# Performance work log

Measured on AMD Instinct MI355X. Metric: run time of the kernel, lower is better.

The kernel has to match this reference:

```python
import jax, jax.numpy as jnp
import numpy as np

N = 50000   # nodes
E = 200000  # edges (avg degree ~4, pose-graph-like sparsity)
F_IN = 512
NEG_SLOPE = 0.01  # F.leaky_relu default


def _softmax_aggr(src_feat, dst, num_nodes):
    # torch_geometric SoftmaxAggregation(t=1): per-destination, per-feature
    # alpha = softmax(x_j), out = sum_j alpha * x_j
    m = jax.ops.segment_max(src_feat, dst, num_segments=num_nodes)  # [N,F]
    m = jnp.where(jnp.isfinite(m), m, 0.0)  # empty segments -> -inf guard
    e = jnp.exp(src_feat - m[dst])                                   # [E,F]
    denom = jax.ops.segment_sum(e, dst, num_segments=num_nodes)      # [N,F]
    num = jax.ops.segment_sum(e * src_feat, dst, num_segments=num_nodes)
    return num / jnp.maximum(denom, 1e-16)  # 0 for isolated nodes


def setup_inputs() -> dict:
    key = jax.random.key(0)
    ks = jax.random.split(key, 9)
    inp = {
        "x": jax.random.normal(ks[0], (N, F_IN), dtype=jnp.float32),
        "W1_rel": jax.random.normal(ks[1], (513, 256), dtype=jnp.float32) * 0.04,
        "b1_rel": jnp.zeros((256,), dtype=jnp.float32),
        "W1_root": jax.random.normal(ks[2], (513, 256), dtype=jnp.float32) * 0.04,
        "W2_rel": jax.random.normal(ks[3], (257, 64), dtype=jnp.float32) * 0.06,
        "b2_rel": jnp.zeros((64,), dtype=jnp.float32),
        "W2_root": jax.random.normal(ks[4], (257, 64), dtype=jnp.float32) * 0.06,
        "Wp": jax.random.normal(ks[5], (65, 3), dtype=jnp.float32) * 0.1,
        "bp": jnp.zeros((3,), dtype=jnp.float32),
        "Wr": jax.random.normal(ks[6], (65, 4), dtype=jnp.float32) * 0.1,
        "br": jnp.zeros((4,), dtype=jnp.float32),
        "edge_index": jax.random.randint(ks[7], (2, E), 0, N, dtype=jnp.int64),
    }
    return inp


def reference(x, W1_rel, b1_rel, W1_root, W2_rel, b2_rel, W2_root,
              Wp, bp, Wr, br, edge_index):
    src, dst = edge_index[0], edge_index[1]
    node_index = jnp.arange(x.shape[0], dtype=x.dtype)[:, None]  # [N,1]

    # dropout is identity in eval mode
    h = jnp.concatenate([x, node_index], axis=1)  # [N,513]

    # GraphConv(513,256, aggr='softmax'): lin_rel(softmax_aggr(x_j)) + lin_root(x)
    agg1 = _softmax_aggr(h[src], dst, x.shape[0])               # [N,513]
    h = agg1 @ W1_rel + b1_rel + h @ W1_root                     # [N,256]
    h = jnp.where(h >= 0, h, NEG_SLOPE * h)

    h = jnp.concatenate([h, node_index], axis=1)  # [N,257]

    # GraphConv(257,64) default aggr='add'
    agg2 = jax.ops.segment_sum(h[src], dst, num_segments=x.shape[0])  # [N,257]
    h = agg2 @ W2_rel + b2_rel + h @ W2_root                           # [N,64]
    h = jnp.where(h >= 0, h, NEG_SLOPE * h)

    h = jnp.concatenate([h, node_index], axis=1)  # [N,65]

    position = h @ Wp + bp                         # [N,3]
    rotation = h @ Wr + br                         # [N,4]
    norm = jnp.linalg.norm(rotation, axis=1, keepdims=True)
    rotation = rotation / jnp.maximum(norm, 1e-12)  # F.normalize

    return jnp.concatenate([position, rotation], axis=1)  # [N,7]
```

## Files before the change

kernel.cpp:

```cpp
#include <hip/hip_runtime.h>

#define NNODES 50000
#define NEDGES 200000
#define NSCANB ((NNODES + 255) / 256)

typedef short  bf16x8 __attribute__((ext_vector_type(8)));
typedef float  f32x4  __attribute__((ext_vector_type(4)));
typedef unsigned int u32x4 __attribute__((ext_vector_type(4)));

__device__ __forceinline__ unsigned short f2bf(float f) {
    union { float f; unsigned int u; } c; c.f = f;
    unsigned int r = c.u + 0x7fffu + ((c.u >> 16) & 1u);
    return (unsigned short)(r >> 16);
}
__device__ __forceinline__ float bflo(unsigned int v) {
    union { unsigned int u; float f; } c; c.u = v << 16;
    return c.f;
}
__device__ __forceinline__ float bfhi(unsigned int v) {
    union { unsigned int u; float f; } c; c.u = v & 0xffff0000u;
    return c.f;
}

#define PREP_B1 (256 * 1024)
#define PREP_B2 (64 * 512)
#define PREP_XC (NNODES * 64)
__global__ __launch_bounds__(256) void k_prepcount(const float* __restrict__ x,
                                                   const float* __restrict__ W1_rel,
                                                   const float* __restrict__ W1_root,
                                                   const float* __restrict__ W2_rel,
                                                   const float* __restrict__ W2_root,
                                                   const int* __restrict__ ei,
                                                   int* __restrict__ deg,
                                                   unsigned short* __restrict__ Bt1,
                                                   unsigned short* __restrict__ Bt2,
                                                   unsigned short* __restrict__ xb) {
    const int gtid = blockIdx.x * 256 + threadIdx.x;
    const int GS = gridDim.x * 256;
    for (int e = gtid; e < NEDGES; e += GS) atomicAdd(&deg[ei[NEDGES + e]], 1);
    for (int i = gtid; i < PREP_B1; i += GS) {
        int n = i >> 10, k = i & 1023;
        float v = (k < 512) ? W1_rel[k * 256 + n] : W1_root[(k - 512) * 256 + n];
        Bt1[i] = f2bf(v);
    }
    for (int i = gtid; i < PREP_B2; i += GS) {
        int n = i >> 9, k = i & 511;
        float v = (k < 256) ? W2_rel[k * 64 + n] : W2_root[(k - 256) * 64 + n];
        Bt2[i] = f2bf(v);
    }
    for (int i = gtid; i < PREP_XC; i += GS) {
        int n = i >> 6, c8 = (i & 63) * 8;
        const float* xp = x + (size_t)n * 512 + c8;
        float4 a = *(const float4*)xp;
        float4 bb = *(const float4*)(xp + 4);
        unsigned short o[8];
        o[0] = f2bf(a.x); o[1] = f2bf(a.y); o[2] = f2bf(a.z); o[3] = f2bf(a.w);
        o[4] = f2bf(bb.x); o[5] = f2bf(bb.y); o[6] = f2bf(bb.z); o[7] = f2bf(bb.w);
        *(u32x4*)(xb + (size_t)n * 512 + c8) = *(const u32x4*)o;
    }
}

__global__ __launch_bounds__(256) void k_scanA(const int* __restrict__ deg,
                                               int* __restrict__ rs,
                                               int* __restrict__ partials) {
    __shared__ int sm[256];
    int t = threadIdx.x, i = blockIdx.x * 256 + t;
    int v = (i < NNODES) ? deg[i] : 0;
    sm[t] = v;
    __syncthreads();
#pragma unroll
    for (int off = 1; off < 256; off <<= 1) {
        int u = (t >= off) ? sm[t - off] : 0;
        __syncthreads();
        sm[t] += u;
        __syncthreads();
    }
    if (i < NNODES) rs[i] = sm[t] - v;
    if (t == 255) partials[blockIdx.x] = sm[255];
}

__global__ __launch_bounds__(256) void k_scanC2(int* __restrict__ rs,
                                                const int* __restrict__ partials,
                                                int* __restrict__ cursor) {
    __shared__ int sm[256];
    int t = threadIdx.x, b = blockIdx.x;
    sm[t] = (t < b && t < NSCANB) ? partials[t] : 0;
    __syncthreads();
#pragma unroll
    for (int off = 128; off; off >>= 1) {
        if (t < off) sm[t] += sm[t + off];
        __syncthreads();
    }
    int off0 = sm[0];
    int i = b * 256 + t;
    if (i < NNODES) {
        int rv = rs[i] + off0;
        rs[i] = rv;
        cursor[i] = rv;
    }
    if (i == 0) rs[NNODES] = NEDGES;
}

__global__ void k_scatter(const int* __restrict__ ei, int* __restrict__ cursor,
                          int* __restrict__ srcs) {
    int e = blockIdx.x * 256 + threadIdx.x;
    if (e < NEDGES) {
        int d = ei[NEDGES + e];
        int p = atomicAdd(&cursor[d], 1);
        srcs[p] = ei[e];
    }
}

__global__ __launch_bounds__(256) void k_agg1(const unsigned short* __restrict__ xb,
                                              const int* __restrict__ rs,
                                              const int* __restrict__ srcs,
                                              unsigned short* __restrict__ AggBuf) {
    int wv = threadIdx.x >> 6;
    int lane = threadIdx.x & 63;
    int n = blockIdx.x * 4 + wv;
    int e0 = rs[n], e1 = rs[n + 1];
    float nu[8], de[8];
#pragma unroll
    for (int j = 0; j < 8; ++j) { nu[j] = 0.f; de[j] = 0.f; }

    auto accum = [&](u32x4 r) {
#pragma unroll
        for (int p = 0; p < 4; ++p) {
            float v0 = bflo(r[p]), v1 = bfhi(r[p]);
            float E0 = __expf(v0), E1 = __expf(v1);
            de[2 * p] += E0; nu[2 * p] += E0 * v0;
            de[2 * p + 1] += E1; nu[2 * p + 1] += E1 * v1;
        }
    };

    int e = e0;
    for (; e + 3 < e1; e += 4) {
        int s0 = srcs[e], s1 = srcs[e + 1], s2 = srcs[e + 2], s3 = srcs[e + 3];
        u32x4 r0 = *(const u32x4*)(xb + (size_t)s0 * 512 + lane * 8);
        u32x4 r1 = *(const u32x4*)(xb + (size_t)s1 * 512 + lane * 8);
        u32x4 r2 = *(const u32x4*)(xb + (size_t)s2 * 512 + lane * 8);
        u32x4 r3 = *(const u32x4*)(xb + (size_t)s3 * 512 + lane * 8);
        accum(r0); accum(r1); accum(r2); accum(r3);
    }
    if (e + 1 < e1) {
        int s0 = srcs[e], s1 = srcs[e + 1];
        u32x4 r0 = *(const u32x4*)(xb + (size_t)s0 * 512 + lane * 8);
        u32x4 r1 = *(const u32x4*)(xb + (size_t)s1 * 512 + lane * 8);
        accum(r0); accum(r1);
        e += 2;
    }
    if (e < e1) {
        u32x4 r0 = *(const u32x4*)(xb + (size_t)srcs[e] * 512 + lane * 8);
        accum(r0);
    }
    unsigned short o[8];
#pragma unroll
    for (int j = 0; j < 8; ++j) o[j] = f2bf(nu[j] / fmaxf(de[j], 1e-16f));
    *(u32x4*)(AggBuf + (size_t)n * 512 + lane * 8) = *(const u32x4*)o;
}

__global__ __launch_bounds__(256) void k_agg2(const int* __restrict__ rs,
                                              const int* __restrict__ srcs,
                                              const unsigned short* __restrict__ H1,
                                              unsigned short* __restrict__ Seg) {
    int wv = threadIdx.x >> 6;
    int lane = threadIdx.x & 63;
    int n = blockIdx.x * 4 + wv;
    int e0 = rs[n], e1 = rs[n + 1];
    float a[4] = {0.f, 0.f, 0.f, 0.f};

    auto accum = [&](uint2 r) {
        a[0] += bflo(r.x); a[1] += bfhi(r.x);
        a[2] += bflo(r.y); a[3] += bfhi(r.y);
    };

    int e = e0;
    for (; e + 3 < e1; e += 4) {
        int s0 = srcs[e], s1 = srcs[e + 1], s2 = srcs[e + 2], s3 = srcs[e + 3];
        uint2 r0 = *(const uint2*)(H1 + (size_t)s0 * 256 + lane * 4);
        uint2 r1 = *(const uint2*)(H1 + (size_t)s1 * 256 + lane * 4);
        uint2 r2 = *(const uint2*)(H1 + (size_t)s2 * 256 + lane * 4);
        uint2 r3 = *(const uint2*)(H1 + (size_t)s3 * 256 + lane * 4);
        accum(r0); accum(r1); accum(r2); accum(r3);
    }
    if (e + 1 < e1) {
        int s0 = srcs[e], s1 = srcs[e + 1];
        uint2 r0 = *(const uint2*)(H1 + (size_t)s0 * 256 + lane * 4);
        uint2 r1 = *(const uint2*)(H1 + (size_t)s1 * 256 + lane * 4);
        accum(r0); accum(r1);
        e += 2;
    }
    if (e < e1) {
        uint2 r0 = *(const uint2*)(H1 + (size_t)srcs[e] * 256 + lane * 4);
        accum(r0);
    }
    uint2 o;
    o.x = (unsigned int)f2bf(a[0]) | ((unsigned int)f2bf(a[1]) << 16);
    o.y = (unsigned int)f2bf(a[2]) | ((unsigned int)f2bf(a[3]) << 16);
    *(uint2*)(Seg + (size_t)n * 256 + lane * 4) = o;
}

__global__ __launch_bounds__(256) void k_gemm1(const unsigned short* __restrict__ A1,
                                               const unsigned short* __restrict__ A2,
                                               const unsigned short* __restrict__ Bt,
                                               const int* __restrict__ rs,
                                               const int* __restrict__ srcs,
                                               const float* __restrict__ r1,
                                               const float* __restrict__ r2,
                                               const float* __restrict__ bias,
                                               unsigned short* __restrict__ outp) {
    constexpr int BM = 64, BN = 128, BK = 64;
    __shared__ __align__(16) unsigned short As[2][BM * BK];
    __shared__ __align__(16) unsigned short Bs[2][BN * BK];
    __shared__ float s1t[BM];

    const int tid = threadIdx.x;
    const int w = tid >> 6;
    const int lane = tid & 63;
    const int lm = lane & 15;
    const int quad = lane >> 4;
    const int wr = w >> 1;
    const int wc = w & 1;
    const int rowbase = blockIdx.y * BM;
    const int colbase = blockIdx.x * BN;
    const int wrow = wr * 32;
    const int wcol = wc * 64;

    const int rsub = lane >> 3;
    const int csw = (lane & 7) ^ rsub;

    f32x4 acc[2][4];
#pragma unroll
    for (int mi = 0; mi < 2; ++mi)
#pragma unroll
        for (int ni = 0; ni < 4; ++ni) acc[mi][ni] = (f32x4){0.f, 0.f, 0.f, 0.f};

    auto stage = [&](unsigned short* Asb, unsigned short* Bsb, int kt) {
        const unsigned short* Ab = (kt < 512) ? A1 : A2;
        int kof = (kt < 512) ? kt : kt - 512;
#pragma unroll
        for (int l = 0; l < 2; ++l) {
            int r = w * 16 + l * 8;
            int gr = rowbase + r + rsub;
            if (gr >= NNODES) gr = NNODES - 1;
            const unsigned short* gp = Ab + (size_t)gr * 512 + kof + csw * 8;
            __builtin_amdgcn_global_load_lds(
                (const __attribute__((address_space(1))) void*)gp,
                (__attribute__((address_space(3))) void*)(Asb + r * BK), 16, 0, 0);
        }
#pragma unroll
        for (int l = 0; l < 4; ++l) {
            int r = w * 32 + l * 8;
            const unsigned short* gp = Bt + (size_t)(colbase + r + rsub) * 1024 + kt + csw * 8;
            __builtin_amdgcn_global_load_lds(
                (const __attribute__((address_space(1))) void*)gp,
                (__attribute__((address_space(3))) void*)(Bsb + r * BK), 16, 0, 0);
        }
    };

    auto compute = [&](const unsigned short* Asb, const unsigned short* Bsb) {
#pragma unroll
        for (int kk = 0; kk < BK; kk += 32) {
            const int kidx = (kk >> 3) + quad;
            const int phys = kidx ^ (lm & 7);
            bf16x8 af[2], bfr[4];
#pragma unroll
            for (int mi = 0; mi < 2; ++mi)
                af[mi] = __builtin_bit_cast(bf16x8,
                    *(const u32x4*)(Asb + (wrow + mi * 16 + lm) * BK + phys * 8));
#pragma unroll
            for (int ni = 0; ni < 4; ++ni)
                bfr[ni] = __builtin_bit_cast(bf16x8,
                    *(const u32x4*)(Bsb + (wcol + ni * 16 + lm) * BK + phys * 8));
#pragma unroll
            for (int mi = 0; mi < 2; ++mi)
#pragma unroll
                for (int ni = 0; ni < 4; ++ni)
                    acc[mi][ni] = __builtin_amdgcn_mfma_f32_16x16x32_bf16(
                        af[mi], bfr[ni], acc[mi][ni], 0, 0, 0);
        }
    };

    stage(As[0], Bs[0], 0);
#pragma unroll 1
    for (int t = 0; t < 16; t += 2) {
        stage(As[1], Bs[1], (t + 1) * BK);
        asm volatile("s_waitcnt vmcnt(6)" ::: "memory");
        __builtin_amdgcn_s_barrier();
        __builtin_amdgcn_sched_barrier(0);
        compute(As[0], Bs[0]);
        __builtin_amdgcn_s_barrier();
        if (t + 2 < 16) {
            stage(As[0], Bs[0], (t + 2) * BK);
            asm volatile("s_waitcnt vmcnt(6)" ::: "memory");
        } else {
            asm volatile("s_waitcnt vmcnt(0)" ::: "memory");
        }
        __builtin_amdgcn_s_barrier();
        __builtin_amdgcn_sched_barrier(0);
        compute(As[1], Bs[1]);
        __builtin_amdgcn_s_barrier();
    }

    if (tid < BM) {
        int grow = rowbase + tid;
        float r_ = 0.f;
        if (grow < NNODES) {
            int e0 = rs[grow], e1 = rs[grow + 1];
            float m = -INFINITY, d = 0.f, q = 0.f;
            for (int e = e0; e < e1; ++e) {
                float v = (float)srcs[e];
                float nm = fmaxf(m, v);
                float sc = __expf(m - nm), ee = __expf(v - nm);
                d = d * sc + ee;
                q = q * sc + ee * v;
                m = nm;
            }
            r_ = q / fmaxf(d, 1e-16f);
        }
        s1t[tid] = r_;
    }
    __syncthreads();

#pragma unroll
    for (int ni = 0; ni < 4; ++ni) {
        int gc = colbase + wcol + ni * 16 + lm;
        float r1v = r1[gc], r2v = r2[gc], bv = bias[gc];
#pragma unroll
        for (int mi = 0; mi < 2; ++mi) {
#pragma unroll
            for (int r = 0; r < 4; ++r) {
                int lrow = wrow + mi * 16 + quad * 4 + r;
                int grow = rowbase + lrow;
                if (grow < NNODES) {
                    float v = acc[mi][ni][r] + s1t[lrow] * r1v + (float)grow * r2v + bv;
                    v = (v >= 0.f) ? v : 0.01f * v;
                    outp[(size_t)grow * 256 + gc] = f2bf(v);
                }
            }
        }
    }
}

__global__ __launch_bounds__(256) void k_gemm2h(const unsigned short* __restrict__ A1,
                                                const unsigned short* __restrict__ A2,
                                                const unsigned short* __restrict__ Bt,
                                                const int* __restrict__ rs,
                                                const int* __restrict__ srcs,
                                                const float* __restrict__ r1,
                                                const float* __restrict__ r2,
                                                const float* __restrict__ bias,
                                                const float* __restrict__ Wp,
                                                const float* __restrict__ bp,
                                                const float* __restrict__ Wr,
                                                const float* __restrict__ br,
                                                float* __restrict__ out) {
    constexpr int BM = 64, BN = 64, BK = 64;
    __shared__ __align__(16) unsigned short As[BM * BK];
    __shared__ __align__(16) unsigned short Bs[BN * BK];
    __shared__ float h2t[BM * 65];
    __shared__ float s1t[BM];

    const int tid = threadIdx.x;
    const int w = tid >> 6;
    const int lane = tid & 63;
    const int lm = lane & 15;
    const int quad = lane >> 4;
    const int rowbase = blockIdx.x * BM;
    const int wrow = w * 16;

    const int rsub = lane >> 3;
    const int csw = (lane & 7) ^ rsub;

    f32x4 acc[4];
#pragma unroll
    for (int ni = 0; ni < 4; ++ni) acc[ni] = (f32x4){0.f, 0.f, 0.f, 0.f};

    for (int kt = 0; kt < 512; kt += BK) {
        const unsigned short* Ab = (kt < 256) ? A1 : A2;
        int kof = (kt < 256) ? kt : kt - 256;
#pragma unroll
        for (int l = 0; l < 2; ++l) {
            int r = w * 16 + l * 8;
            int gr = rowbase + r + rsub;
            if (gr >= NNODES) gr = NNODES - 1;
            const unsigned short* gp = Ab + (size_t)gr * 256 + kof + csw * 8;
            __builtin_amdgcn_global_load_lds(
                (const __attribute__((address_space(1))) void*)gp,
                (__attribute__((address_space(3))) void*)(As + r * BK), 16, 0, 0);
        }
#pragma unroll
        for (int l = 0; l < 2; ++l) {
            int r = w * 16 + l * 8;
            const unsigned short* gp = Bt + (size_t)(r + rsub) * 512 + kt + csw * 8;
            __builtin_amdgcn_global_load_lds(
                (const __attribute__((address_space(1))) void*)gp,
                (__attribute__((address_space(3))) void*)(Bs + r * BK), 16, 0, 0);
        }
        __syncthreads();
#pragma unroll
        for (int kk = 0; kk < BK; kk += 32) {
            const int kidx = (kk >> 3) + quad;
            const int phys = kidx ^ (lm & 7);
            bf16x8 af;
            af = __builtin_bit_cast(bf16x8,
                *(const u32x4*)(As + (wrow + lm) * BK + phys * 8));
            bf16x8 bfr[4];
#pragma unroll
            for (int ni = 0; ni < 4; ++ni)
                bfr[ni] = __builtin_bit_cast(bf16x8,
                    *(const u32x4*)(Bs + (ni * 16 + lm) * BK + phys * 8));
#pragma unroll
            for (int ni = 0; ni < 4; ++ni)
                acc[ni] = __builtin_amdgcn_mfma_f32_16x16x32_bf16(
                    af, bfr[ni], acc[ni], 0, 0, 0);
        }
        __syncthreads();
    }

    if (tid < BM) {
        int grow = rowbase + tid;
        float si = 0.f;
        if (grow < NNODES) {
            int e0 = rs[grow], e1 = rs[grow + 1];
            for (int e = e0; e < e1; ++e) si += (float)srcs[e];
        }
        s1t[tid] = si;
    }
    __syncthreads();

#pragma unroll
    for (int ni = 0; ni < 4; ++ni) {
        int gc = ni * 16 + lm;
        float r1v = r1[gc], r2v = r2[gc], bv = bias[gc];
#pragma unroll
        for (int r = 0; r < 4; ++r) {
            int lrow = wrow + quad * 4 + r;
            int grow = rowbase + lrow;
            float v = acc[ni][r] + s1t[lrow] * r1v + (float)grow * r2v + bv;
            v = (v >= 0.f) ? v : 0.01f * v;
            h2t[lrow * 65 + gc] = v;
        }
    }
    __syncthreads();

    if (tid < BM) {
        int grow = rowbase + tid;
        if (grow < NNODES) {
            const float* hv = h2t + tid * 65;
            float idx = (float)grow;
            float p0 = 0.f, p1 = 0.f, p2 = 0.f;
            float r0 = 0.f, r1a = 0.f, r2a = 0.f, r3 = 0.f;
#pragma unroll 8
            for (int c = 0; c < 64; ++c) {
                float v = hv[c];
                p0 += v * Wp[c * 3 + 0];
                p1 += v * Wp[c * 3 + 1];
                p2 += v * Wp[c * 3 + 2];
                r0 += v * Wr[c * 4 + 0];
                r1a += v * Wr[c * 4 + 1];
                r2a += v * Wr[c * 4 + 2];
                r3 += v * Wr[c * 4 + 3];
            }
            p0 += idx * Wp[64 * 3 + 0] + bp[0];
            p1 += idx * Wp[64 * 3 + 1] + bp[1];
            p2 += idx * Wp[64 * 3 + 2] + bp[2];
            r0 += idx * Wr[64 * 4 + 0] + br[0];
            r1a += idx * Wr[64 * 4 + 1] + br[1];
            r2a += idx * Wr[64 * 4 + 2] + br[2];
            r3 += idx * Wr[64 * 4 + 3] + br[3];
            float nrm = fmaxf(sqrtf(r0 * r0 + r1a * r1a + r2a * r2a + r3 * r3), 1e-12f);
            float* op = out + (size_t)grow * 7;
            op[0] = p0; op[1] = p1; op[2] = p2;
            op[3] = r0 / nrm; op[4] = r1a / nrm; op[5] = r2a / nrm; op[6] = r3 / nrm;
        }
    }
}

extern "C" void kernel_launch(void* const* d_in, const int* in_sizes, int n_in,
                              void* d_out, int out_size, void* d_ws, size_t ws_size,
                              hipStream_t stream) {
    const float* x       = (const float*)d_in[0];
    const float* W1_rel  = (const float*)d_in[1];
    const float* b1      = (const float*)d_in[2];
    const float* W1_root = (const float*)d_in[3];
    const float* W2_rel  = (const float*)d_in[4];
    const float* b2      = (const float*)d_in[5];
    const float* W2_root = (const float*)d_in[6];
    const float* Wp      = (const float*)d_in[7];
    const float* bp      = (const float*)d_in[8];
    const float* Wr      = (const float*)d_in[9];
    const float* br      = (const float*)d_in[10];
    const int*   ei      = (const int*)d_in[11];
    float* out = (float*)d_out;

    char* ws = (char*)d_ws;
    size_t off = 0;
    auto alloc = [&](size_t bytes) {
        size_t o = off;
        off = (off + bytes + 255) & ~(size_t)255;
        return (void*)(ws + o);
    };
    int*   deg       = (int*)alloc(NNODES * 4);
    int*   cursor    = (int*)alloc(NNODES * 4);
    int*   row_start = (int*)alloc((NNODES + 1) * 4);
    int*   srcs      = (int*)alloc(NEDGES * 4);
    int*   partials  = (int*)alloc(NSCANB * 4);
    unsigned short* xb     = (unsigned short*)alloc((size_t)NNODES * 512 * 2);
    unsigned short* AggBuf = (unsigned short*)alloc((size_t)NNODES * 512 * 2);
    unsigned short* H1     = (unsigned short*)alloc((size_t)NNODES * 256 * 2);
    unsigned short* Seg    = (unsigned short*)alloc((size_t)NNODES * 256 * 2);
    unsigned short* Bt1    = (unsigned short*)alloc(256 * 1024 * 2);
    unsigned short* Bt2    = (unsigned short*)alloc(64 * 512 * 2);

    hipMemsetAsync(deg, 0, NNODES * 4, stream);

    k_prepcount<<<2048, 256, 0, stream>>>(
        x, W1_rel, W1_root, W2_rel, W2_root, ei, deg, Bt1, Bt2, xb);

    k_scanA<<<NSCANB, 256, 0, stream>>>(deg, row_start, partials);
    k_scanC2<<<NSCANB, 256, 0, stream>>>(row_start, partials, cursor);
    k_scatter<<<(NEDGES + 255) / 256, 256, 0, stream>>>(ei, cursor, srcs);

    k_agg1<<<NNODES / 4, 256, 0, stream>>>(xb, row_start, srcs, AggBuf);

    k_gemm1<<<dim3(2, (NNODES + 63) / 64), 256, 0, stream>>>(
        AggBuf, xb, Bt1, row_start, srcs, W1_rel + 512 * 256, W1_root + 512 * 256, b1, H1);

    k_agg2<<<NNODES / 4, 256, 0, stream>>>(row_start, srcs, H1, Seg);

    k_gemm2h<<<(NNODES + 63) / 64, 256, 0, stream>>>(
        Seg, H1, Bt2, row_start, srcs, W2_rel + 256 * 64, W2_root + 256 * 64, b2,
        Wp, bp, Wr, br, out);
}
```

Measured before the change: 339.7 us.

## Reorder layer-2 as transform-then-aggregate and fuse the head into aggregation

```diff
diff --git a/kernel.cpp b/kernel.cpp
--- a/kernel.cpp
+++ b/kernel.cpp
@@ -13,6 +13,10 @@
     unsigned int r = c.u + 0x7fffu + ((c.u >> 16) & 1u);
     return (unsigned short)(r >> 16);
 }
+__device__ __forceinline__ float bf2f(unsigned short h) {
+    union { unsigned int u; float f; } c; c.u = ((unsigned int)h) << 16;
+    return c.f;
+}
 __device__ __forceinline__ float bflo(unsigned int v) {
     union { unsigned int u; float f; } c; c.u = v << 16;
     return c.f;
@@ -23,7 +27,7 @@
 }
 
 #define PREP_B1 (256 * 1024)
-#define PREP_B2 (64 * 512)
+#define PREP_B2 (128 * 256)
 #define PREP_XC (NNODES * 64)
 __global__ __launch_bounds__(256) void k_prepcount(const float* __restrict__ x,
                                                    const float* __restrict__ W1_rel,
@@ -44,8 +48,8 @@
         Bt1[i] = f2bf(v);
     }
     for (int i = gtid; i < PREP_B2; i += GS) {
-        int n = i >> 9, k = i & 511;
-        float v = (k < 256) ? W2_rel[k * 64 + n] : W2_root[(k - 256) * 64 + n];
+        int n = i >> 8, k = i & 255;
+        float v = (n < 64) ? W2_rel[k * 64 + n] : W2_root[k * 64 + (n - 64)];
         Bt2[i] = f2bf(v);
     }
     for (int i = gtid; i < PREP_XC; i += GS) {
@@ -157,47 +161,6 @@
 #pragma unroll
     for (int j = 0; j < 8; ++j) o[j] = f2bf(nu[j] / fmaxf(de[j], 1e-16f));
     *(u32x4*)(AggBuf + (size_t)n * 512 + lane * 8) = *(const u32x4*)o;
-}
-
-__global__ __launch_bounds__(256) void k_agg2(const int* __restrict__ rs,
-                                              const int* __restrict__ srcs,
-                                              const unsigned short* __restrict__ H1,
-                                              unsigned short* __restrict__ Seg) {
-    int wv = threadIdx.x >> 6;
-    int lane = threadIdx.x & 63;
-    int n = blockIdx.x * 4 + wv;
-    int e0 = rs[n], e1 = rs[n + 1];
-    float a[4] = {0.f, 0.f, 0.f, 0.f};
-
-    auto accum = [&](uint2 r) {
-        a[0] += bflo(r.x); a[1] += bfhi(r.x);
-        a[2] += bflo(r.y); a[3] += bfhi(r.y);
-    };
-
-    int e = e0;
-    for (; e + 3 < e1; e += 4) {
-        int s0 = srcs[e], s1 = srcs[e + 1], s2 = srcs[e + 2], s3 = srcs[e + 3];
-        uint2 r0 = *(const uint2*)(H1 + (size_t)s0 * 256 + lane * 4);
-        uint2 r1 = *(const uint2*)(H1 + (size_t)s1 * 256 + lane * 4);
-        uint2 r2 = *(const uint2*)(H1 + (size_t)s2 * 256 + lane * 4);
-        uint2 r3 = *(const uint2*)(H1 + (size_t)s3 * 256 + lane * 4);
-        accum(r0); accum(r1); accum(r2); accum(r3);
-    }
-    if (e + 1 < e1) {
-        int s0 = srcs[e], s1 = srcs[e + 1];
-        uint2 r0 = *(const uint2*)(H1 + (size_t)s0 * 256 + lane * 4);
-        uint2 r1 = *(const uint2*)(H1 + (size_t)s1 * 256 + lane * 4);
-        accum(r0); accum(r1);
-        e += 2;
-    }
-    if (e < e1) {
-        uint2 r0 = *(const uint2*)(H1 + (size_t)srcs[e] * 256 + lane * 4);
-        accum(r0);
-    }
-    uint2 o;
-    o.x = (unsigned int)f2bf(a[0]) | ((unsigned int)f2bf(a[1]) << 16);
-    o.y = (unsigned int)f2bf(a[2]) | ((unsigned int)f2bf(a[3]) << 16);
-    *(uint2*)(Seg + (size_t)n * 256 + lane * 4) = o;
 }
 
 __global__ __launch_bounds__(256) void k_gemm1(const unsigned short* __restrict__ A1,
@@ -342,57 +305,49 @@
     }
 }
 
-__global__ __launch_bounds__(256) void k_gemm2h(const unsigned short* __restrict__ A1,
-                                                const unsigned short* __restrict__ A2,
-                                                const unsigned short* __restrict__ Bt,
-                                                const int* __restrict__ rs,
-                                                const int* __restrict__ srcs,
-                                                const float* __restrict__ r1,
-                                                const float* __restrict__ r2,
-                                                const float* __restrict__ bias,
-                                                const float* __restrict__ Wp,
-                                                const float* __restrict__ bp,
-                                                const float* __restrict__ Wr,
-                                                const float* __restrict__ br,
-                                                float* __restrict__ out) {
-    constexpr int BM = 64, BN = 64, BK = 64;
+__global__ __launch_bounds__(256) void k_gemm2(const unsigned short* __restrict__ H1,
+                                               const unsigned short* __restrict__ Bt,
+                                               unsigned short* __restrict__ GR) {
+    constexpr int BM = 64, BN = 128, BK = 64;
     __shared__ __align__(16) unsigned short As[BM * BK];
     __shared__ __align__(16) unsigned short Bs[BN * BK];
-    __shared__ float h2t[BM * 65];
-    __shared__ float s1t[BM];
 
     const int tid = threadIdx.x;
     const int w = tid >> 6;
     const int lane = tid & 63;
     const int lm = lane & 15;
     const int quad = lane >> 4;
+    const int wr = w >> 1;
+    const int wc = w & 1;
     const int rowbase = blockIdx.x * BM;
-    const int wrow = w * 16;
+    const int wrow = wr * 32;
+    const int wcol = wc * 64;
 
     const int rsub = lane >> 3;
     const int csw = (lane & 7) ^ rsub;
 
-    f32x4 acc[4];
-#pragma unroll
-    for (int ni = 0; ni < 4; ++ni) acc[ni] = (f32x4){0.f, 0.f, 0.f, 0.f};
-
-    for (int kt = 0; kt < 512; kt += BK) {
-        const unsigned short* Ab = (kt < 256) ? A1 : A2;
-        int kof = (kt < 256) ? kt : kt - 256;
+    f32x4 acc[2][4];
+#pragma unroll
+    for (int mi = 0; mi < 2; ++mi)
+#pragma unroll
+        for (int ni = 0; ni < 4; ++ni) acc[mi][ni] = (f32x4){0.f, 0.f, 0.f, 0.f};
+
+#pragma unroll 1
+    for (int kt = 0; kt < 256; kt += BK) {
 #pragma unroll
         for (int l = 0; l < 2; ++l) {
             int r = w * 16 + l * 8;
             int gr = rowbase + r + rsub;
             if (gr >= NNODES) gr = NNODES - 1;
-            const unsigned short* gp = Ab + (size_t)gr * 256 + kof + csw * 8;
+            const unsigned short* gp = H1 + (size_t)gr * 256 + kt + csw * 8;
             __builtin_amdgcn_global_load_lds(
                 (const __attribute__((address_space(1))) void*)gp,
                 (__attribute__((address_space(3))) void*)(As + r * BK), 16, 0, 0);
         }
 #pragma unroll
-        for (int l = 0; l < 2; ++l) {
-            int r = w * 16 + l * 8;
-            const unsigned short* gp = Bt + (size_t)(r + rsub) * 512 + kt + csw * 8;
+        for (int l = 0; l < 4; ++l) {
+            int r = w * 32 + l * 8;
+            const unsigned short* gp = Bt + (size_t)(r + rsub) * 256 + kt + csw * 8;
             __builtin_amdgcn_global_load_lds(
                 (const __attribute__((address_space(1))) void*)gp,
                 (__attribute__((address_space(3))) void*)(Bs + r * BK), 16, 0, 0);
@@ -402,79 +357,114 @@
         for (int kk = 0; kk < BK; kk += 32) {
             const int kidx = (kk >> 3) + quad;
             const int phys = kidx ^ (lm & 7);
-            bf16x8 af;
-            af = __builtin_bit_cast(bf16x8,
-                *(const u32x4*)(As + (wrow + lm) * BK + phys * 8));
-            bf16x8 bfr[4];
+            bf16x8 af[2], bfr[4];
+#pragma unroll
+            for (int mi = 0; mi < 2; ++mi)
+                af[mi] = __builtin_bit_cast(bf16x8,
+                    *(const u32x4*)(As + (wrow + mi * 16 + lm) * BK + phys * 8));
 #pragma unroll
             for (int ni = 0; ni < 4; ++ni)
                 bfr[ni] = __builtin_bit_cast(bf16x8,
-                    *(const u32x4*)(Bs + (ni * 16 + lm) * BK + phys * 8));
-#pragma unroll
-            for (int ni = 0; ni < 4; ++ni)
-                acc[ni] = __builtin_amdgcn_mfma_f32_16x16x32_bf16(
-                    af, bfr[ni], acc[ni], 0, 0, 0);
+                    *(const u32x4*)(Bs + (wcol + ni * 16 + lm) * BK + phys * 8));
+#pragma unroll
+            for (int mi = 0; mi < 2; ++mi)
+#pragma unroll
+                for (int ni = 0; ni < 4; ++ni)
+                    acc[mi][ni] = __builtin_amdgcn_mfma_f32_16x16x32_bf16(
+                        af[mi], bfr[ni], acc[mi][ni], 0, 0, 0);
         }
         __syncthreads();
     }
 
-    if (tid < BM) {
-        int grow = rowbase + tid;
-        float si = 0.f;
-        if (grow < NNODES) {
-            int e0 = rs[grow], e1 = rs[grow + 1];
-            for (int e = e0; e < e1; ++e) si += (float)srcs[e];
-        }
-        s1t[tid] = si;
-    }
-    __syncthreads();
-
 #pragma unroll
     for (int ni = 0; ni < 4; ++ni) {
-        int gc = ni * 16 + lm;
-        float r1v = r1[gc], r2v = r2[gc], bv = bias[gc];
-#pragma unroll
-        for (int r = 0; r < 4; ++r) {
-            int lrow = wrow + quad * 4 + r;
-            int grow = rowbase + lrow;
-            float v = acc[ni][r] + s1t[lrow] * r1v + (float)grow * r2v + bv;
-            v = (v >= 0.f) ? v : 0.01f * v;
-            h2t[lrow * 65 + gc] = v;
-        }
-    }
-    __syncthreads();
-
-    if (tid < BM) {
-        int grow = rowbase + tid;
-        if (grow < NNODES) {
-            const float* hv = h2t + tid * 65;
-            float idx = (float)grow;
-            float p0 = 0.f, p1 = 0.f, p2 = 0.f;
-            float r0 = 0.f, r1a = 0.f, r2a = 0.f, r3 = 0.f;
-#pragma unroll 8
-            for (int c = 0; c < 64; ++c) {
-                float v = hv[c];
-                p0 += v * Wp[c * 3 + 0];
-                p1 += v * Wp[c * 3 + 1];
-                p2 += v * Wp[c * 3 + 2];
-                r0 += v * Wr[c * 4 + 0];
-                r1a += v * Wr[c * 4 + 1];
-                r2a += v * Wr[c * 4 + 2];
-                r3 += v * Wr[c * 4 + 3];
+        int gc = wcol + ni * 16 + lm;
+#pragma unroll
+        for (int mi = 0; mi < 2; ++mi) {
+#pragma unroll
+            for (int r = 0; r < 4; ++r) {
+                int lrow = wrow + mi * 16 + quad * 4 + r;
+                int grow = rowbase + lrow;
+                if (grow < NNODES)
+                    GR[(size_t)grow * 128 + gc] = f2bf(acc[mi][ni][r]);
             }
-            p0 += idx * Wp[64 * 3 + 0] + bp[0];
-            p1 += idx * Wp[64 * 3 + 1] + bp[1];
-            p2 += idx * Wp[64 * 3 + 2] + bp[2];
-            r0 += idx * Wr[64 * 4 + 0] + br[0];
-            r1a += idx * Wr[64 * 4 + 1] + br[1];
-            r2a += idx * Wr[64 * 4 + 2] + br[2];
-            r3 += idx * Wr[64 * 4 + 3] + br[3];
-            float nrm = fmaxf(sqrtf(r0 * r0 + r1a * r1a + r2a * r2a + r3 * r3), 1e-12f);
-            float* op = out + (size_t)grow * 7;
-            op[0] = p0; op[1] = p1; op[2] = p2;
-            op[3] = r0 / nrm; op[4] = r1a / nrm; op[5] = r2a / nrm; op[6] = r3 / nrm;
-        }
-    }
+        }
+    }
+}
+
+__global__ __launch_bounds__(256) void k_agg2h(const int* __restrict__ rs,
+                                               const int* __restrict__ srcs,
+                                               const unsigned short* __restrict__ GR,
+                                               const float* __restrict__ r1,
+                                               const float* __restrict__ r2,
+                                               const float* __restrict__ bias,
+                                               const float* __restrict__ Wp,
+                                               const float* __restrict__ bp,
+                                               const float* __restrict__ Wr,
+                                               const float* __restrict__ br,
+                                               float* __restrict__ out) {
+    const int wv = threadIdx.x >> 6;
+    const int lane = threadIdx.x & 63;
+    const int n = blockIdx.x * 4 + wv;
+    const int e0 = rs[n], e1 = rs[n + 1];
+
+    float g = 0.f, si = 0.f;
+    int e = e0;
+    for (; e + 3 < e1; e += 4) {
+        int s0 = srcs[e], s1 = srcs[e + 1], s2 = srcs[e + 2], s3 = srcs[e + 3];
+        float g0 = bf2f(GR[(size_t)s0 * 128 + lane]);
+        float g1 = bf2f(GR[(size_t)s1 * 128 + lane]);
+        float g2 = bf2f(GR[(size_t)s2 * 128 + lane]);
+        float g3 = bf2f(GR[(size_t)s3 * 128 + lane]);
+        g += (g0 + g1) + (g2 + g3);
+        si += (float)(s0 + s1) + (float)(s2 + s3);
+    }
+    if (e + 1 < e1) {
+        int s0 = srcs[e], s1 = srcs[e + 1];
+        g += bf2f(GR[(size_t)s0 * 128 + lane]) + bf2f(GR[(size_t)s1 * 128 + lane]);
+        si += (float)(s0 + s1);
+        e += 2;
+    }
+    if (e < e1) {
+        int s0 = srcs[e];
+        g += bf2f(GR[(size_t)s0 * 128 + lane]);
+        si += (float)s0;
+    }
+
+    float h2 = g + si * r1[lane] + bf2f(GR[(size_t)n * 128 + 64 + lane])
+             + (float)n * r2[lane] + bias[lane];
+    h2 = (h2 >= 0.f) ? h2 : 0.01f * h2;
+
+    float p0 = h2 * Wp[lane * 3 + 0];
+    float p1 = h2 * Wp[lane * 3 + 1];
+    float p2 = h2 * Wp[lane * 3 + 2];
+    float q0 = h2 * Wr[lane * 4 + 0];
+    float q1 = h2 * Wr[lane * 4 + 1];
+    float q2 = h2 * Wr[lane * 4 + 2];
+    float q3 = h2 * Wr[lane * 4 + 3];
+#pragma unroll
+    for (int m = 1; m < 64; m <<= 1) {
+        p0 += __shfl_xor(p0, m);
+        p1 += __shfl_xor(p1, m);
+        p2 += __shfl_xor(p2, m);
+        q0 += __shfl_xor(q0, m);
+        q1 += __shfl_xor(q1, m);
+        q2 += __shfl_xor(q2, m);
+        q3 += __shfl_xor(q3, m);
+    }
+    const float idx = (float)n;
+    p0 += idx * Wp[64 * 3 + 0] + bp[0];
+    p1 += idx * Wp[64 * 3 + 1] + bp[1];
+    p2 += idx * Wp[64 * 3 + 2] + bp[2];
+    q0 += idx * Wr[64 * 4 + 0] + br[0];
+    q1 += idx * Wr[64 * 4 + 1] + br[1];
+    q2 += idx * Wr[64 * 4 + 2] + br[2];
+    q3 += idx * Wr[64 * 4 + 3] + br[3];
+    float nrm = fmaxf(sqrtf(q0 * q0 + q1 * q1 + q2 * q2 + q3 * q3), 1e-12f);
+    float o = (lane == 0) ? p0 : (lane == 1) ? p1 : (lane == 2) ? p2
+            : (lane == 3) ? q0 / nrm : (lane == 4) ? q1 / nrm
+            : (lane == 5) ? q2 / nrm : q3 / nrm;
+    if (lane < 7) out[(size_t)n * 7 + lane] = o;
 }
 
 extern "C" void kernel_launch(void* const* d_in, const int* in_sizes, int n_in,
@@ -509,9 +499,9 @@
     unsigned short* xb     = (unsigned short*)alloc((size_t)NNODES * 512 * 2);
     unsigned short* AggBuf = (unsigned short*)alloc((size_t)NNODES * 512 * 2);
     unsigned short* H1     = (unsigned short*)alloc((size_t)NNODES * 256 * 2);
-    unsigned short* Seg    = (unsigned short*)alloc((size_t)NNODES * 256 * 2);
+    unsigned short* GR     = (unsigned short*)alloc((size_t)NNODES * 128 * 2);
     unsigned short* Bt1    = (unsigned short*)alloc(256 * 1024 * 2);
-    unsigned short* Bt2    = (unsigned short*)alloc(64 * 512 * 2);
+    unsigned short* Bt2    = (unsigned short*)alloc(128 * 256 * 2);
 
     hipMemsetAsync(deg, 0, NNODES * 4, stream);
 
@@ -527,9 +517,9 @@
     k_gemm1<<<dim3(2, (NNODES + 63) / 64), 256, 0, stream>>>(
         AggBuf, xb, Bt1, row_start, srcs, W1_rel + 512 * 256, W1_root + 512 * 256, b1, H1);
 
-    k_agg2<<<NNODES / 4, 256, 0, stream>>>(row_start, srcs, H1, Seg);
-
-    k_gemm2h<<<(NNODES + 63) / 64, 256, 0, stream>>>(
-        Seg, H1, Bt2, row_start, srcs, W2_rel + 256 * 64, W2_root + 256 * 64, b2,
+    k_gemm2<<<(NNODES + 63) / 64, 256, 0, stream>>>(H1, Bt2, GR);
+
+    k_agg2h<<<NNODES / 4, 256, 0, stream>>>(
+        row_start, srcs, GR, W2_rel + 256 * 64, W2_root + 256 * 64, b2,
         Wp, bp, Wr, br, out);
 }
```

Result: no change. 335.8 us (-1.2%).
